# Optimization experiments

Hardware: AMD Instinct MI355X
Metric: run time of the kernel (lower is better)

## Reference

```python
import jax, jax.numpy as jnp
import numpy as np

B, S, D = 4096, 200, 64
EPS = 1e-3  # keras BatchNormalization default epsilon

def setup_inputs() -> dict:
    key = jax.random.key(0)
    ks = jax.random.split(key, 8)
    return {
        "em": jax.random.normal(ks[0], (B, D), jnp.float32),
        "eu": jax.random.normal(ks[1], (B, D), jnp.float32),
        "Xu": jax.random.normal(ks[2], (B, S, D), jnp.float32),
        "W1": jax.random.normal(ks[3], (4 * D, 64), jnp.float32) * 0.05,
        "b1": jnp.zeros((64,), jnp.float32),
        "W2": jax.random.normal(ks[4], (64, 32), jnp.float32) * 0.1,
        "b2": jnp.zeros((32,), jnp.float32),
        "W3": jax.random.normal(ks[5], (32, 1), jnp.float32) * 0.1,
        "b3": jnp.zeros((1,), jnp.float32),
        "gamma": jnp.ones((2 * D,), jnp.float32),
        "beta": jnp.zeros((2 * D,), jnp.float32),
        "mov_mean": jnp.zeros((2 * D,), jnp.float32),
        "mov_var": jnp.ones((2 * D,), jnp.float32),
    }

def reference(em, eu, Xu, W1, b1, W2, b2, W3, b3, gamma, beta, mov_mean, mov_var):
    # DIN attention: query = em tiled over seq, key = value = Xu
    q = jnp.broadcast_to(em[:, None, :], Xu.shape)            # [B,S,D]
    info = jnp.concatenate([q, Xu, q - Xu, q * Xu], axis=-1)  # [B,S,4D]
    h = jax.nn.relu(info @ W1 + b1)                           # [B,S,64]
    h = jax.nn.relu(h @ W2 + b2)                              # [B,S,32]
    logits = (h @ W3 + b3)[..., 0]                            # [B,S]
    w = jax.nn.softmax(logits, axis=-1)                       # [B,S]
    pooled = jnp.einsum('bs,bsd->bd', w, Xu)                  # [B,D]
    info_all = jnp.concatenate([pooled, em], axis=-1)         # [B,2D]
    bn = (info_all - mov_mean) * jax.lax.rsqrt(mov_var + EPS) * gamma + beta
    return jnp.concatenate([bn, eu], axis=-1)                 # [B,2D+Du]
```

## Files before the change

kernel.cpp:

```cpp
#include <hip/hip_runtime.h>
#include <hip/hip_bf16.h>
#include <math.h>

typedef __bf16 bf16_t;
typedef bf16_t bf16x4 __attribute__((ext_vector_type(4)));
typedef bf16_t bf16x8 __attribute__((ext_vector_type(8)));
typedef float  f32x4  __attribute__((ext_vector_type(4)));

#define SEQ 200
#define DD  64
#define NT  13

#define MFMA(a, b, c) __builtin_amdgcn_mfma_f32_16x16x32_bf16((a), (b), (c), 0, 0, 0)

__global__ __launch_bounds__(256) void prep_kernel(
    const float* __restrict__ em, const float* __restrict__ W1,
    const float* __restrict__ b1, const float* __restrict__ W2,
    bf16_t* __restrict__ Wbc, bf16_t* __restrict__ W1dt,
    bf16_t* __restrict__ W2t, float* __restrict__ Q)
{
  const int tid = threadIdx.x;
  if (blockIdx.x == 0) {
    for (int i = tid; i < 64 * 64; i += 256) {
      int n = i >> 6, k = i & 63;
      Wbc[i]  = (bf16_t)(W1[(64 + k) * 64 + n] - W1[(128 + k) * 64 + n]);
      W1dt[i] = (bf16_t)(W1[(192 + k) * 64 + n]);
    }
    for (int i = tid; i < 32 * 64; i += 256) {
      int n = i >> 6, k = i & 63;
      W2t[i] = (bf16_t)(W2[k * 32 + n]);
    }
  } else {
    int b = (blockIdx.x - 1) * 4 + (tid >> 6);
    int n = tid & 63;
    float acc = b1[n];
    for (int d = 0; d < 64; ++d)
      acc += em[(size_t)b * 64 + d] * (W1[d * 64 + n] + W1[(128 + d) * 64 + n]);
    Q[(size_t)b * 64 + n] = acc;
  }
}

__global__ __launch_bounds__(256, 4) void din_kernel(
    const float* __restrict__ em, const float* __restrict__ eu,
    const float* __restrict__ Xu, const float* __restrict__ b2,
    const float* __restrict__ W3, const float* __restrict__ gam,
    const float* __restrict__ bet, const float* __restrict__ mmean,
    const float* __restrict__ mvar, const bf16_t* __restrict__ Wbc,
    const bf16_t* __restrict__ W1dt, const bf16_t* __restrict__ W2t,
    const float* __restrict__ Q, float* __restrict__ out)
{
  __shared__ __align__(16) unsigned char lds[4 * 4416];

  const int tid  = threadIdx.x;
  const int wid  = tid >> 6;
  const int lane = tid & 63;
  const int g    = lane >> 4;
  const int l16  = lane & 15;
  const int b    = blockIdx.x * 4 + wid;

  bf16_t* h1   = (bf16_t*)(lds + wid * 4416);
  float*  pool = (float*)(lds + wid * 4416);
  float*  lam  = (float*)(lds + wid * 4416 + 4352);

  const bf16x8* Wbc8  = (const bf16x8*)Wbc;
  const bf16x8* W1dt8 = (const bf16x8*)W1dt;
  const bf16x8* W2t8  = (const bf16x8*)W2t;

  float eml[2][8];
  #pragma unroll
  for (int c = 0; c < 2; ++c) {
    float4 e0 = *(const float4*)&em[(size_t)b * DD + 32 * c + 8 * g];
    float4 e1 = *(const float4*)&em[(size_t)b * DD + 32 * c + 8 * g + 4];
    eml[c][0] = e0.x; eml[c][1] = e0.y; eml[c][2] = e0.z; eml[c][3] = e0.w;
    eml[c][4] = e1.x; eml[c][5] = e1.y; eml[c][6] = e1.z; eml[c][7] = e1.w;
  }
  bf16x8 bB[4][2];
  #pragma unroll
  for (int nt = 0; nt < 4; ++nt) {
    int n = nt * 16 + l16;
    #pragma unroll
    for (int c = 0; c < 2; ++c) {
      bf16x8 wbc = Wbc8[n * 8 + 4 * c + g];
      bf16x8 w1d = W1dt8[n * 8 + 4 * c + g];
      #pragma unroll
      for (int j = 0; j < 8; ++j)
        bB[nt][c][j] = (bf16_t)((float)wbc[j] + eml[c][j] * (float)w1d[j]);
    }
  }
  bf16x8 bW2[2][2];
  #pragma unroll
  for (int c = 0; c < 2; ++c)
    #pragma unroll
    for (int u = 0; u < 2; ++u)
      bW2[c][u] = W2t8[(16 * u + l16) * 8 + 4 * c + g];

  float qv[4];
  #pragma unroll
  for (int nt = 0; nt < 4; ++nt) qv[nt] = Q[(size_t)b * DD + nt * 16 + l16];
  const float b2v0 = b2[l16], b2v1 = b2[16 + l16];
  const float w3v0 = W3[l16], w3v1 = W3[16 + l16];

  float m = -INFINITY, l = 0.f;
  float pacc[2][8];
  #pragma unroll
  for (int c = 0; c < 2; ++c)
    #pragma unroll
    for (int j = 0; j < 8; ++j) pacc[c][j] = 0.f;

  const float* Xbase = Xu + (size_t)b * SEQ * DD;

  for (int t = 0; t < NT; ++t) {
    const int s = 16 * t + l16;
    bf16x8 xf[2];
    if (s < SEQ) {
      const float* Xr = Xbase + (size_t)s * DD;
      #pragma unroll
      for (int c = 0; c < 2; ++c) {
        float4 x0 = *(const float4*)&Xr[32 * c + 8 * g];
        float4 x1 = *(const float4*)&Xr[32 * c + 8 * g + 4];
        xf[c][0] = (bf16_t)x0.x; xf[c][1] = (bf16_t)x0.y;
        xf[c][2] = (bf16_t)x0.z; xf[c][3] = (bf16_t)x0.w;
        xf[c][4] = (bf16_t)x1.x; xf[c][5] = (bf16_t)x1.y;
        xf[c][6] = (bf16_t)x1.z; xf[c][7] = (bf16_t)x1.w;
      }
    } else {
      #pragma unroll
      for (int c = 0; c < 2; ++c)
        #pragma unroll
        for (int j = 0; j < 8; ++j) xf[c][j] = (bf16_t)0.f;
    }

    f32x4 a1[4];
    #pragma unroll
    for (int nt = 0; nt < 4; ++nt) {
      f32x4 a = {0.f, 0.f, 0.f, 0.f};
      a = MFMA(xf[0], bB[nt][0], a);
      a = MFMA(xf[1], bB[nt][1], a);
      a1[nt] = a;
    }
    #pragma unroll
    for (int nt = 0; nt < 4; ++nt)
      #pragma unroll
      for (int r = 0; r < 4; ++r) {
        float v = a1[nt][r] + qv[nt];
        v = v > 0.f ? v : 0.f;
        h1[(4 * g + r) * 72 + nt * 16 + l16] = (bf16_t)v;
      }

    bf16x8 h0 = *(const bf16x8*)&h1[l16 * 72 + 8 * g];
    bf16x8 h1f = *(const bf16x8*)&h1[l16 * 72 + 32 + 8 * g];
    f32x4 a20 = {0.f, 0.f, 0.f, 0.f}, a21 = {0.f, 0.f, 0.f, 0.f};
    a20 = MFMA(h0, bW2[0][0], a20);
    a20 = MFMA(h1f, bW2[1][0], a20);
    a21 = MFMA(h0, bW2[0][1], a21);
    a21 = MFMA(h1f, bW2[1][1], a21);

    #pragma unroll
    for (int r = 0; r < 4; ++r) {
      float p0 = fmaxf(a20[r] + b2v0, 0.f) * w3v0;
      float p1 = fmaxf(a21[r] + b2v1, 0.f) * w3v1;
      float pr = p0 + p1;
      pr += __shfl_xor(pr, 1);
      pr += __shfl_xor(pr, 2);
      pr += __shfl_xor(pr, 4);
      pr += __shfl_xor(pr, 8);
      if (l16 == 0) {
        int row = 4 * g + r;
        lam[row] = (16 * t + row < SEQ) ? pr : -INFINITY;
      }
    }
    float lv = lam[l16];
    float mt = lv;
    mt = fmaxf(mt, __shfl_xor(mt, 1));
    mt = fmaxf(mt, __shfl_xor(mt, 2));
    mt = fmaxf(mt, __shfl_xor(mt, 4));
    mt = fmaxf(mt, __shfl_xor(mt, 8));

    float mn = fmaxf(m, mt);
    float alpha = __expf(m - mn);
    float e = __expf(lv - mn);
    float es = e;
    es += __shfl_xor(es, 1);
    es += __shfl_xor(es, 2);
    es += __shfl_xor(es, 4);
    es += __shfl_xor(es, 8);
    l = l * alpha + es;
    #pragma unroll
    for (int c = 0; c < 2; ++c)
      #pragma unroll
      for (int j = 0; j < 8; ++j)
        pacc[c][j] = pacc[c][j] * alpha + e * (float)xf[c][j];
    m = mn;
  }

  {
    f32x4 p;
    p[0] = pacc[0][0]; p[1] = pacc[0][1]; p[2] = pacc[0][2]; p[3] = pacc[0][3];
    *(f32x4*)&pool[l16 * 68 + 8 * g] = p;
    p[0] = pacc[0][4]; p[1] = pacc[0][5]; p[2] = pacc[0][6]; p[3] = pacc[0][7];
    *(f32x4*)&pool[l16 * 68 + 8 * g + 4] = p;
    p[0] = pacc[1][0]; p[1] = pacc[1][1]; p[2] = pacc[1][2]; p[3] = pacc[1][3];
    *(f32x4*)&pool[l16 * 68 + 32 + 8 * g] = p;
    p[0] = pacc[1][4]; p[1] = pacc[1][5]; p[2] = pacc[1][6]; p[3] = pacc[1][7];
    *(f32x4*)&pool[l16 * 68 + 32 + 8 * g + 4] = p;
  }
  float ps = 0.f;
  #pragma unroll
  for (int r = 0; r < 16; ++r) ps += pool[r * 68 + lane];
  const float pooled = ps * (1.f / l);

  const size_t ob = (size_t)b * 192;
  out[ob + lane] =
      (pooled - mmean[lane]) * rsqrtf(mvar[lane] + 1e-3f) * gam[lane] + bet[lane];
  float emv = em[(size_t)b * DD + lane];
  out[ob + 64 + lane] =
      (emv - mmean[64 + lane]) * rsqrtf(mvar[64 + lane] + 1e-3f) * gam[64 + lane] +
      bet[64 + lane];
  out[ob + 128 + lane] = eu[(size_t)b * DD + lane];
}

extern "C" void kernel_launch(void* const* d_in, const int* in_sizes, int n_in,
                              void* d_out, int out_size, void* d_ws, size_t ws_size,
                              hipStream_t stream) {
  const float* em = (const float*)d_in[0];
  const float* eu = (const float*)d_in[1];
  const float* Xu = (const float*)d_in[2];
  const float* W1 = (const float*)d_in[3];
  const float* b1 = (const float*)d_in[4];
  const float* W2 = (const float*)d_in[5];
  const float* b2 = (const float*)d_in[6];
  const float* W3 = (const float*)d_in[7];
  const float* ga = (const float*)d_in[9];
  const float* be = (const float*)d_in[10];
  const float* mm = (const float*)d_in[11];
  const float* mv = (const float*)d_in[12];
  int B = in_sizes[0] / DD;

  float*  Q    = (float*)d_ws;
  bf16_t* Wbc  = (bf16_t*)((char*)d_ws + (size_t)B * 64 * 4);
  bf16_t* W1dt = Wbc  + 64 * 64;
  bf16_t* W2t  = W1dt + 64 * 64;

  prep_kernel<<<1 + B / 4, 256, 0, stream>>>(em, W1, b1, W2, Wbc, W1dt, W2t, Q);
  din_kernel<<<B / 4, 256, 0, stream>>>(em, eu, Xu, b2, W3, ga, be, mm, mv,
                                        Wbc, W1dt, W2t, Q, (float*)d_out);
}
```

Baseline: 339.3 us.

## Assign one batch row per block and stage its sequence in LDS cooperatively

Each block now handles a single batch element instead of four. All 256 threads load the 200x64 Xu slice with coalesced float4 reads, convert it to bf16, and store it in shared memory. The four waves then split the 13 sequence tiles, each running its own online softmax, and the partial max, sum and pooled vectors are merged across waves through shared memory. The aim is more parallelism per batch row and better global load coalescing, at the cost of more blocks, block-wide barriers and larger LDS use (about 30KB per block), which may reduce occupancy.

Measured after the change: 344.9 us. No clear change (+1.7%).

```diff
diff --git a/kernel.cpp b/kernel.cpp
--- a/kernel.cpp
+++ b/kernel.cpp
@@ -9,7 +9,7 @@
 
 #define SEQ 200
 #define DD  64
-#define NT  13
+#define RS  72
 
 #define MFMA(a, b, c) __builtin_amdgcn_mfma_f32_16x16x32_bf16((a), (b), (c), 0, 0, 0)
 
@@ -49,42 +49,71 @@
     const bf16_t* __restrict__ W1dt, const bf16_t* __restrict__ W2t,
     const float* __restrict__ Q, float* __restrict__ out)
 {
-  __shared__ __align__(16) unsigned char lds[4 * 4416];
+  __shared__ __align__(16) bf16_t A[208 * RS];
+  __shared__ float lam[4][16];
+  __shared__ float wavebuf[4][DD];
+  __shared__ float mlbuf[4][2];
 
   const int tid  = threadIdx.x;
   const int wid  = tid >> 6;
   const int lane = tid & 63;
   const int g    = lane >> 4;
   const int l16  = lane & 15;
-  const int b    = blockIdx.x * 4 + wid;
-
-  bf16_t* h1   = (bf16_t*)(lds + wid * 4416);
-  float*  pool = (float*)(lds + wid * 4416);
-  float*  lam  = (float*)(lds + wid * 4416 + 4352);
+  const int b    = blockIdx.x;
+
+  for (int i = tid; i < 8 * DD; i += 256) {
+    int r = SEQ + (i >> 6), c = i & 63;
+    A[r * RS + c] = (bf16_t)0.f;
+  }
+
+  const float4* Xr = (const float4*)(Xu + (size_t)b * SEQ * DD);
+  #pragma unroll 1
+  for (int k0 = 0; k0 < 12; k0 += 4) {
+    float4 x[4];
+    #pragma unroll
+    for (int u = 0; u < 4; ++u) x[u] = Xr[tid + 256 * (k0 + u)];
+    #pragma unroll
+    for (int u = 0; u < 4; ++u) {
+      int v = tid + 256 * (k0 + u);
+      bf16x4 xa;
+      xa[0] = (bf16_t)x[u].x; xa[1] = (bf16_t)x[u].y;
+      xa[2] = (bf16_t)x[u].z; xa[3] = (bf16_t)x[u].w;
+      *(bf16x4*)&A[(v >> 4) * RS + (v & 15) * 4] = xa;
+    }
+  }
+  if (tid < 128) {
+    float4 x = Xr[3072 + tid];
+    int v = 3072 + tid;
+    bf16x4 xa;
+    xa[0] = (bf16_t)x.x; xa[1] = (bf16_t)x.y;
+    xa[2] = (bf16_t)x.z; xa[3] = (bf16_t)x.w;
+    *(bf16x4*)&A[(v >> 4) * RS + (v & 15) * 4] = xa;
+  }
 
   const bf16x8* Wbc8  = (const bf16x8*)Wbc;
   const bf16x8* W1dt8 = (const bf16x8*)W1dt;
   const bf16x8* W2t8  = (const bf16x8*)W2t;
-
-  float eml[2][8];
-  #pragma unroll
-  for (int c = 0; c < 2; ++c) {
-    float4 e0 = *(const float4*)&em[(size_t)b * DD + 32 * c + 8 * g];
-    float4 e1 = *(const float4*)&em[(size_t)b * DD + 32 * c + 8 * g + 4];
-    eml[c][0] = e0.x; eml[c][1] = e0.y; eml[c][2] = e0.z; eml[c][3] = e0.w;
-    eml[c][4] = e1.x; eml[c][5] = e1.y; eml[c][6] = e1.z; eml[c][7] = e1.w;
-  }
   bf16x8 bB[4][2];
-  #pragma unroll
-  for (int nt = 0; nt < 4; ++nt) {
-    int n = nt * 16 + l16;
+  {
+    float eml[2][8];
     #pragma unroll
     for (int c = 0; c < 2; ++c) {
-      bf16x8 wbc = Wbc8[n * 8 + 4 * c + g];
-      bf16x8 w1d = W1dt8[n * 8 + 4 * c + g];
+      float4 e0 = *(const float4*)&em[(size_t)b * DD + 32 * c + 8 * g];
+      float4 e1 = *(const float4*)&em[(size_t)b * DD + 32 * c + 8 * g + 4];
+      eml[c][0] = e0.x; eml[c][1] = e0.y; eml[c][2] = e0.z; eml[c][3] = e0.w;
+      eml[c][4] = e1.x; eml[c][5] = e1.y; eml[c][6] = e1.z; eml[c][7] = e1.w;
+    }
+    #pragma unroll
+    for (int nt = 0; nt < 4; ++nt) {
+      int n = nt * 16 + l16;
       #pragma unroll
-      for (int j = 0; j < 8; ++j)
-        bB[nt][c][j] = (bf16_t)((float)wbc[j] + eml[c][j] * (float)w1d[j]);
+      for (int c = 0; c < 2; ++c) {
+        bf16x8 wbc = Wbc8[n * 8 + 4 * c + g];
+        bf16x8 w1d = W1dt8[n * 8 + 4 * c + g];
+        #pragma unroll
+        for (int j = 0; j < 8; ++j)
+          bB[nt][c][j] = (bf16_t)((float)wbc[j] + eml[c][j] * (float)w1d[j]);
+      }
     }
   }
   bf16x8 bW2[2][2];
@@ -100,42 +129,24 @@
   const float b2v0 = b2[l16], b2v1 = b2[16 + l16];
   const float w3v0 = W3[l16], w3v1 = W3[16 + l16];
 
+  __syncthreads();
+
   float m = -INFINITY, l = 0.f;
-  float pacc[2][8];
-  #pragma unroll
-  for (int c = 0; c < 2; ++c)
-    #pragma unroll
-    for (int j = 0; j < 8; ++j) pacc[c][j] = 0.f;
-
-  const float* Xbase = Xu + (size_t)b * SEQ * DD;
-
-  for (int t = 0; t < NT; ++t) {
-    const int s = 16 * t + l16;
-    bf16x8 xf[2];
-    if (s < SEQ) {
-      const float* Xr = Xbase + (size_t)s * DD;
-      #pragma unroll
-      for (int c = 0; c < 2; ++c) {
-        float4 x0 = *(const float4*)&Xr[32 * c + 8 * g];
-        float4 x1 = *(const float4*)&Xr[32 * c + 8 * g + 4];
-        xf[c][0] = (bf16_t)x0.x; xf[c][1] = (bf16_t)x0.y;
-        xf[c][2] = (bf16_t)x0.z; xf[c][3] = (bf16_t)x0.w;
-        xf[c][4] = (bf16_t)x1.x; xf[c][5] = (bf16_t)x1.y;
-        xf[c][6] = (bf16_t)x1.z; xf[c][7] = (bf16_t)x1.w;
-      }
-    } else {
-      #pragma unroll
-      for (int c = 0; c < 2; ++c)
-        #pragma unroll
-        for (int j = 0; j < 8; ++j) xf[c][j] = (bf16_t)0.f;
-    }
+  float pacc[16];
+  #pragma unroll
+  for (int i = 0; i < 16; ++i) pacc[i] = 0.f;
+
+  for (int t = wid; t < 13; t += 4) {
+    const int rb = (16 * t + l16) * RS + 8 * g;
+    bf16x8 xa0 = *(const bf16x8*)&A[rb];
+    bf16x8 xa1 = *(const bf16x8*)&A[rb + 32];
 
     f32x4 a1[4];
     #pragma unroll
     for (int nt = 0; nt < 4; ++nt) {
       f32x4 a = {0.f, 0.f, 0.f, 0.f};
-      a = MFMA(xf[0], bB[nt][0], a);
-      a = MFMA(xf[1], bB[nt][1], a);
+      a = MFMA(xa0, bB[nt][0], a);
+      a = MFMA(xa1, bB[nt][1], a);
       a1[nt] = a;
     }
     #pragma unroll
@@ -144,11 +155,11 @@
       for (int r = 0; r < 4; ++r) {
         float v = a1[nt][r] + qv[nt];
         v = v > 0.f ? v : 0.f;
-        h1[(4 * g + r) * 72 + nt * 16 + l16] = (bf16_t)v;
+        A[(16 * t + 4 * g + r) * RS + nt * 16 + l16] = (bf16_t)v;
       }
 
-    bf16x8 h0 = *(const bf16x8*)&h1[l16 * 72 + 8 * g];
-    bf16x8 h1f = *(const bf16x8*)&h1[l16 * 72 + 32 + 8 * g];
+    bf16x8 h0  = *(const bf16x8*)&A[rb];
+    bf16x8 h1f = *(const bf16x8*)&A[rb + 32];
     f32x4 a20 = {0.f, 0.f, 0.f, 0.f}, a21 = {0.f, 0.f, 0.f, 0.f};
     a20 = MFMA(h0, bW2[0][0], a20);
     a20 = MFMA(h1f, bW2[1][0], a20);
@@ -166,19 +177,19 @@
       pr += __shfl_xor(pr, 8);
       if (l16 == 0) {
         int row = 4 * g + r;
-        lam[row] = (16 * t + row < SEQ) ? pr : -INFINITY;
+        lam[wid][row] = (16 * t + row < SEQ) ? pr : -INFINITY;
       }
     }
-    float lv = lam[l16];
+    float lv = lam[wid][l16];
     float mt = lv;
     mt = fmaxf(mt, __shfl_xor(mt, 1));
     mt = fmaxf(mt, __shfl_xor(mt, 2));
     mt = fmaxf(mt, __shfl_xor(mt, 4));
     mt = fmaxf(mt, __shfl_xor(mt, 8));
 
-    float mn = fmaxf(m, mt);
+    float mn    = fmaxf(m, mt);
     float alpha = __expf(m - mn);
-    float e = __expf(lv - mn);
+    float e     = __expf(lv - mn);
     float es = e;
     es += __shfl_xor(es, 1);
     es += __shfl_xor(es, 2);
@@ -186,37 +197,52 @@
     es += __shfl_xor(es, 8);
     l = l * alpha + es;
     #pragma unroll
-    for (int c = 0; c < 2; ++c)
-      #pragma unroll
-      for (int j = 0; j < 8; ++j)
-        pacc[c][j] = pacc[c][j] * alpha + e * (float)xf[c][j];
+    for (int j = 0; j < 8; ++j) {
+      pacc[j]     = pacc[j]     * alpha + e * (float)xa0[j];
+      pacc[8 + j] = pacc[8 + j] * alpha + e * (float)xa1[j];
+    }
     m = mn;
   }
 
-  {
-    f32x4 p;
-    p[0] = pacc[0][0]; p[1] = pacc[0][1]; p[2] = pacc[0][2]; p[3] = pacc[0][3];
-    *(f32x4*)&pool[l16 * 68 + 8 * g] = p;
-    p[0] = pacc[0][4]; p[1] = pacc[0][5]; p[2] = pacc[0][6]; p[3] = pacc[0][7];
-    *(f32x4*)&pool[l16 * 68 + 8 * g + 4] = p;
-    p[0] = pacc[1][0]; p[1] = pacc[1][1]; p[2] = pacc[1][2]; p[3] = pacc[1][3];
-    *(f32x4*)&pool[l16 * 68 + 32 + 8 * g] = p;
-    p[0] = pacc[1][4]; p[1] = pacc[1][5]; p[2] = pacc[1][6]; p[3] = pacc[1][7];
-    *(f32x4*)&pool[l16 * 68 + 32 + 8 * g + 4] = p;
-  }
-  float ps = 0.f;
-  #pragma unroll
-  for (int r = 0; r < 16; ++r) ps += pool[r * 68 + lane];
-  const float pooled = ps * (1.f / l);
-
-  const size_t ob = (size_t)b * 192;
-  out[ob + lane] =
-      (pooled - mmean[lane]) * rsqrtf(mvar[lane] + 1e-3f) * gam[lane] + bet[lane];
-  float emv = em[(size_t)b * DD + lane];
-  out[ob + 64 + lane] =
-      (emv - mmean[64 + lane]) * rsqrtf(mvar[64 + lane] + 1e-3f) * gam[64 + lane] +
-      bet[64 + lane];
-  out[ob + 128 + lane] = eu[(size_t)b * DD + lane];
+  #pragma unroll
+  for (int i = 0; i < 16; ++i) {
+    pacc[i] += __shfl_xor(pacc[i], 1);
+    pacc[i] += __shfl_xor(pacc[i], 2);
+    pacc[i] += __shfl_xor(pacc[i], 4);
+    pacc[i] += __shfl_xor(pacc[i], 8);
+  }
+  if (l16 == 0) {
+    #pragma unroll
+    for (int j = 0; j < 8; ++j) {
+      wavebuf[wid][8 * g + j]      = pacc[j];
+      wavebuf[wid][32 + 8 * g + j] = pacc[8 + j];
+    }
+    if (g == 0) { mlbuf[wid][0] = m; mlbuf[wid][1] = l; }
+  }
+  __syncthreads();
+
+  if (tid < 192) {
+    const size_t ob = (size_t)b * 192;
+    float v;
+    if (tid < 64) {
+      float m0 = mlbuf[0][0], m1 = mlbuf[1][0], m2 = mlbuf[2][0], m3 = mlbuf[3][0];
+      float ms = fmaxf(fmaxf(m0, m1), fmaxf(m2, m3));
+      float s0 = __expf(m0 - ms), s1 = __expf(m1 - ms);
+      float s2 = __expf(m2 - ms), s3 = __expf(m3 - ms);
+      float ls = s0 * mlbuf[0][1] + s1 * mlbuf[1][1] +
+                 s2 * mlbuf[2][1] + s3 * mlbuf[3][1];
+      float num = s0 * wavebuf[0][tid] + s1 * wavebuf[1][tid] +
+                  s2 * wavebuf[2][tid] + s3 * wavebuf[3][tid];
+      float pooled = num / ls;
+      v = (pooled - mmean[tid]) * rsqrtf(mvar[tid] + 1e-3f) * gam[tid] + bet[tid];
+    } else if (tid < 128) {
+      float x = em[(size_t)b * DD + (tid - 64)];
+      v = (x - mmean[tid]) * rsqrtf(mvar[tid] + 1e-3f) * gam[tid] + bet[tid];
+    } else {
+      v = eu[(size_t)b * DD + (tid - 128)];
+    }
+    out[ob + tid] = v;
+  }
 }
 
 extern "C" void kernel_launch(void* const* d_in, const int* in_sizes, int n_in,
@@ -242,6 +268,6 @@
   bf16_t* W2t  = W1dt + 64 * 64;
 
   prep_kernel<<<1 + B / 4, 256, 0, stream>>>(em, W1, b1, W2, Wbc, W1dt, W2t, Q);
-  din_kernel<<<B / 4, 256, 0, stream>>>(em, eu, Xu, b2, W3, ga, be, mm, mv,
-                                        Wbc, W1dt, W2t, Q, (float*)d_out);
+  din_kernel<<<B, 256, 0, stream>>>(em, eu, Xu, b2, W3, ga, be, mm, mv,
+                                    Wbc, W1dt, W2t, Q, (float*)d_out);
 }
```
